# Kernel tuning notes

Hardware: AMD Instinct MI355X
Metric: run time of the kernel (lower is better)

The kernel has to match this reference:

```python
import jax, jax.numpy as jnp
import numpy as np

N_NODES = 50000
N_EDGES = 800000
N_GRAPHS = 512


def gcn_conv(x, W, b, src, dst, n_nodes):
    # Standard PyG GCNConv: linear transform, add self-loops, D^-1/2 (A+I) D^-1/2 aggregation.
    x = x @ W  # [N, out]
    loop = jnp.arange(n_nodes, dtype=src.dtype)
    s = jnp.concatenate([src, loop])  # [E+N]
    d = jnp.concatenate([dst, loop])
    deg = jax.ops.segment_sum(jnp.ones_like(d, dtype=x.dtype), d, num_segments=n_nodes)
    dinv = jnp.where(deg > 0, jax.lax.rsqrt(jnp.maximum(deg, 1e-12)), 0.0)
    norm = dinv[s] * dinv[d]  # [E+N]
    msg = x[s] * norm[:, None]  # gather + scale
    out = jax.ops.segment_sum(msg, d, num_segments=n_nodes)  # scatter-add
    return out + b


def setup_inputs() -> dict:
    key = jax.random.key(0)
    ks = jax.random.split(key, 10)
    x = jax.random.normal(ks[0], (N_NODES, 128), dtype=jnp.float32)
    edge_index = jax.random.randint(ks[1], (2, N_EDGES), 0, N_NODES, dtype=jnp.int64)
    batch = jnp.sort(jax.random.randint(ks[2], (N_NODES,), 0, N_GRAPHS, dtype=jnp.int64))
    y = jax.random.randint(ks[3], (N_GRAPHS,), 0, 4, dtype=jnp.int64)
    W1 = jax.random.normal(ks[4], (128, 64), dtype=jnp.float32) * (1.0 / np.sqrt(128))
    b1 = jnp.zeros((64,), dtype=jnp.float32)
    W2 = jax.random.normal(ks[5], (64, 64), dtype=jnp.float32) * (1.0 / np.sqrt(64))
    b2 = jnp.zeros((64,), dtype=jnp.float32)
    Wfc = jax.random.normal(ks[6], (64, 4), dtype=jnp.float32) * (1.0 / np.sqrt(64))
    bfc = jnp.zeros((4,), dtype=jnp.float32)
    return {"x": x, "edge_index": edge_index, "batch": batch, "y": y,
            "W1": W1, "b1": b1, "W2": W2, "b2": b2, "Wfc": Wfc, "bfc": bfc}


def reference(x, edge_index, batch, y, W1, b1, W2, b2, Wfc, bfc):
    src, dst = edge_index[0], edge_index[1]
    h = jax.nn.relu(gcn_conv(x, W1, b1, src, dst, N_NODES))
    h = jax.nn.relu(gcn_conv(h, W2, b2, src, dst, N_NODES))
    # global mean pool over graph ids
    sums = jax.ops.segment_sum(h, batch, num_segments=N_GRAPHS)  # [G, out]
    cnts = jax.ops.segment_sum(jnp.ones((h.shape[0],), h.dtype), batch, num_segments=N_GRAPHS)
    pooled = sums / jnp.maximum(cnts, 1.0)[:, None]
    logits = pooled @ Wfc + bfc
    logp = jax.nn.log_softmax(logits, axis=1)
    return (logp, y)
```

## Files before the change

### kernel.cpp

```cpp
#include <hip/hip_runtime.h>
#include <hip/hip_fp16.h>
#include <math.h>

#define N_NODES 50000
#define N_EDGES 800000
#define N_GRAPHS 512
#define NBKT 196
#define SENT N_NODES
#define CAP_T 6144
#define CAP_S 8192

typedef float v2f __attribute__((ext_vector_type(2)));

#define OFF_BCNT    0u
#define OFF_DINV    1024u
#define OFF_OFFS2   201216u
#define OFF_TMP     601344u
#define OFF_SORTED  5418240u
#define OFF_XS8_1   11840768u
#define OFF_XS8_2   15041024u
#define OFF_HBUF    18241280u

__global__ __launch_bounds__(256) void binA(const int* __restrict__ src, const int* __restrict__ dst,
                                            int* __restrict__ bcnt, unsigned int* __restrict__ tmp,
                                            unsigned int* __restrict__ x1, unsigned int* __restrict__ x2) {
    __shared__ int cnt[256];
    __shared__ int lo[256];
    __shared__ int cnt2[256];
    __shared__ int baseg[256];
    __shared__ unsigned int ldsPK[4096];
    __shared__ int ldsDST[4096];
    int t = threadIdx.x;
    cnt[t] = 0; cnt2[t] = 0;
    if (blockIdx.x == 0) {
        if (t < 16) x1[N_NODES * 16 + t] = 0;
        else if (t < 32) x2[N_NODES * 16 + (t - 16)] = 0;
    }
    __syncthreads();
    int e0 = blockIdx.x * 4096;
    int nE = N_EDGES - e0; if (nE > 4096) nE = 4096;
    int sA[16], dA[16];
#pragma unroll
    for (int i = 0; i < 16; ++i) {
        int e = e0 + i * 256 + t;
        if (e < N_EDGES) {
            sA[i] = src[e];
            dA[i] = dst[e];
            atomicAdd(&cnt[dA[i] >> 8], 1);
        } else dA[i] = -1;
    }
    __syncthreads();
    {
        int v = cnt[t];
        lo[t] = v;
        __syncthreads();
        for (int d = 1; d < 256; d <<= 1) {
            int a = (t >= d) ? lo[t - d] : 0;
            __syncthreads();
            lo[t] += a;
            __syncthreads();
        }
        int ex = lo[t] - v;
        __syncthreads();
        lo[t] = ex;
        baseg[t] = (t < NBKT && v) ? atomicAdd(&bcnt[t], v) : 0;
    }
    __syncthreads();
#pragma unroll
    for (int i = 0; i < 16; ++i) {
        if (dA[i] >= 0) {
            int b = dA[i] >> 8;
            int pl = lo[b] + atomicAdd(&cnt2[b], 1);
            ldsPK[pl] = (unsigned int)sA[i] | ((unsigned int)(dA[i] & 255) << 17);
            ldsDST[pl] = b * CAP_T + baseg[b] + (pl - lo[b]);
        }
    }
    __syncthreads();
    for (int p = t; p < nE; p += 256)
        tmp[ldsDST[p]] = ldsPK[p];
}

__global__ __launch_bounds__(256) void binB2(const unsigned int* __restrict__ tmp,
                                             const int* __restrict__ bcnt,
                                             int* __restrict__ sorted, int2* __restrict__ offs2,
                                             float* __restrict__ dinv) {
    __shared__ int cnt[256];
    __shared__ int scn[256];
    __shared__ int cur[256];
    __shared__ int ldsS[CAP_S];
    int b = blockIdx.x, t = threadIdx.x;
    cnt[t] = 0;
    __syncthreads();
    int m = bcnt[b];
    const unsigned int* tp = tmp + b * CAP_T;
    for (int e = t; e < m; e += 256) atomicAdd(&cnt[tp[e] >> 17], 1);
    __syncthreads();
    int deg = cnt[t];
    int pdeg = (deg + 7) & ~7;
    scn[t] = pdeg;
    __syncthreads();
    for (int d = 1; d < 256; d <<= 1) {
        int a = (t >= d) ? scn[t - d] : 0;
        __syncthreads();
        scn[t] += a;
        __syncthreads();
    }
    int begl = scn[t] - pdeg;
    int ptot = scn[255];
    int node = b * 256 + t;
    if (node < N_NODES) {
        offs2[node] = make_int2(b * CAP_S + begl, b * CAP_S + begl + pdeg);
        dinv[node] = rsqrtf(1.0f + (float)deg);
    }
    cur[t] = begl;
    __syncthreads();
    for (int e = t; e < m; e += 256) {
        unsigned int pk = tp[e];
        int p = atomicAdd(&cur[pk >> 17], 1);
        ldsS[p] = (int)(pk & 0x1FFFFu);
    }
    __syncthreads();
    for (int p = cur[t]; p < begl + pdeg; ++p) ldsS[p] = SENT;
    __syncthreads();
    int4* dst4 = (int4*)(sorted + b * CAP_S);
    const int4* src4 = (const int4*)ldsS;
    for (int p = t; p < (ptot >> 2); p += 256) dst4[p] = src4[p];
}

__global__ __launch_bounds__(256) void gemm1(const float* __restrict__ X, const float* __restrict__ W,
                                             const float* __restrict__ dinv, unsigned int* __restrict__ xs8) {
    __shared__ float sW[128 * 64];
    __shared__ float sX[16 * 132];
    int tid = threadIdx.x;
    {
        const float4* ws = (const float4*)W;
        float4* wd = (float4*)sW;
        for (int i = tid; i < 2048; i += 256) wd[i] = ws[i];
    }
    int row0 = blockIdx.x * 16;
    {
        const float4* xs = (const float4*)(X + row0 * 128);
        for (int i = tid; i < 512; i += 256) {
            int r = i >> 5, q = i & 31;
            *(float4*)&sX[r * 132 + 4 * q] = xs[r * 32 + q];
        }
    }
    __syncthreads();
    int r = tid >> 4;
    int cg = (tid & 15) * 4;
    int row = row0 + r;
    float a0 = 0, a1 = 0, a2 = 0, a3 = 0;
#pragma unroll 8
    for (int k = 0; k < 128; ++k) {
        float xv = sX[r * 132 + k];
        float4 w = *(const float4*)&sW[k * 64 + cg];
        a0 += xv * w.x; a1 += xv * w.y; a2 += xv * w.z; a3 += xv * w.w;
    }
    float s = dinv[row];
    unsigned int pk = 0;
    pk = __builtin_amdgcn_cvt_pk_fp8_f32(a0 * s, a1 * s, pk, false);
    pk = __builtin_amdgcn_cvt_pk_fp8_f32(a2 * s, a3 * s, pk, true);
    xs8[row * 16 + (cg >> 2)] = pk;
}

__global__ __launch_bounds__(256) void gemm2(const float* __restrict__ X, const float* __restrict__ W,
                                             const float* __restrict__ dinv, unsigned int* __restrict__ xs8) {
    __shared__ float sW[64 * 64];
    __shared__ float sX[16][65];
    int tid = threadIdx.x;
    for (int i = tid; i < 64 * 64; i += 256) sW[i] = W[i];
    int row0 = blockIdx.x * 16;
    for (int i = tid; i < 16 * 64; i += 256) {
        int r = i >> 6, k = i & 63;
        sX[r][k] = X[(row0 + r) * 64 + k];
    }
    __syncthreads();
    int r = tid >> 4;
    int cg = (tid & 15) * 4;
    int row = row0 + r;
    float a0 = 0, a1 = 0, a2 = 0, a3 = 0;
#pragma unroll 8
    for (int k = 0; k < 64; ++k) {
        float xv = sX[r][k];
        float4 w = *(const float4*)&sW[k * 64 + cg];
        a0 += xv * w.x; a1 += xv * w.y; a2 += xv * w.z; a3 += xv * w.w;
    }
    float s = dinv[row];
    unsigned int pk = 0;
    pk = __builtin_amdgcn_cvt_pk_fp8_f32(a0 * s, a1 * s, pk, false);
    pk = __builtin_amdgcn_cvt_pk_fp8_f32(a2 * s, a3 * s, pk, true);
    xs8[row * 16 + (cg >> 2)] = pk;
}

#define ADD_ROW(rv) { \
    v2f f0 = __builtin_amdgcn_cvt_pk_f32_fp8((rv).x, false); \
    v2f f1 = __builtin_amdgcn_cvt_pk_f32_fp8((rv).x, true); \
    v2f f2 = __builtin_amdgcn_cvt_pk_f32_fp8((rv).y, false); \
    v2f f3 = __builtin_amdgcn_cvt_pk_f32_fp8((rv).y, true); \
    a0 += f0.x; a1 += f0.y; a2 += f1.x; a3 += f1.y; \
    a4 += f2.x; a5 += f2.y; a6 += f3.x; a7 += f3.y; }

__global__ __launch_bounds__(256) void gather_m(const unsigned char* __restrict__ xs8,
                                                const int2* __restrict__ offs2,
                                                const int* __restrict__ sorted,
                                                const float* __restrict__ dinv,
                                                const float* __restrict__ bias,
                                                float* __restrict__ fout) {
    int wv = blockIdx.x * 4 + (threadIdx.x >> 6);
    int lane = threadIdx.x & 63;
    int sub = lane >> 3, frag = lane & 7;
    int n0 = wv * 4;
    int2 oe = offs2[n0 + (lane < 4 ? lane : 3)];
    int e0 = __shfl(oe.x, 0), e1 = __shfl(oe.x, 1), e2 = __shfl(oe.x, 2);
    int e3 = __shfl(oe.x, 3), e4 = __shfl(oe.y, 3);
    int G   = (e4 - e0) >> 3;
    int nb1 = (e1 - e0) >> 3, nb2 = (e2 - e0) >> 3, nb3 = (e3 - e0) >> 3;
    const int* sb = sorted + e0 + sub;
    int i0 = (0 < G) ? sb[0]  : SENT;
    int i1 = (1 < G) ? sb[8]  : SENT;
    int i2 = (2 < G) ? sb[16] : SENT;
    int i3 = (3 < G) ? sb[24] : SENT;
    float4 bA = *(const float4*)(bias + frag * 8);
    float4 bB = *(const float4*)(bias + frag * 8 + 4);
    int cur = 0;
    uint2 sv = *(const uint2*)(xs8 + n0 * 64 + frag * 8);
    float dv = dinv[n0];
    float a0 = 0, a1 = 0, a2 = 0, a3 = 0, a4 = 0, a5 = 0, a6 = 0, a7 = 0;

#define FLUSH_ADV() { \
    if (sub == 0) ADD_ROW(sv); \
    a0 += __shfl_xor(a0, 8);  a1 += __shfl_xor(a1, 8);  a2 += __shfl_xor(a2, 8);  a3 += __shfl_xor(a3, 8); \
    a4 += __shfl_xor(a4, 8);  a5 += __shfl_xor(a5, 8);  a6 += __shfl_xor(a6, 8);  a7 += __shfl_xor(a7, 8); \
    a0 += __shfl_xor(a0, 16); a1 += __shfl_xor(a1, 16); a2 += __shfl_xor(a2, 16); a3 += __shfl_xor(a3, 16); \
    a4 += __shfl_xor(a4, 16); a5 += __shfl_xor(a5, 16); a6 += __shfl_xor(a6, 16); a7 += __shfl_xor(a7, 16); \
    a0 += __shfl_xor(a0, 32); a1 += __shfl_xor(a1, 32); a2 += __shfl_xor(a2, 32); a3 += __shfl_xor(a3, 32); \
    a4 += __shfl_xor(a4, 32); a5 += __shfl_xor(a5, 32); a6 += __shfl_xor(a6, 32); a7 += __shfl_xor(a7, 32); \
    if (sub == 0) { \
        float4 w0, w1; \
        w0.x = fmaxf(a0 * dv + bA.x, 0.0f); w0.y = fmaxf(a1 * dv + bA.y, 0.0f); \
        w0.z = fmaxf(a2 * dv + bA.z, 0.0f); w0.w = fmaxf(a3 * dv + bA.w, 0.0f); \
        w1.x = fmaxf(a4 * dv + bB.x, 0.0f); w1.y = fmaxf(a5 * dv + bB.y, 0.0f); \
        w1.z = fmaxf(a6 * dv + bB.z, 0.0f); w1.w = fmaxf(a7 * dv + bB.w, 0.0f); \
        float* o = fout + (n0 + cur) * 64 + frag * 8; \
        *(float4*)(o) = w0; *(float4*)(o + 4) = w1; \
    } \
    a0 = a1 = a2 = a3 = a4 = a5 = a6 = a7 = 0.0f; \
    cur++; \
    if (cur < 4) { \
        sv = *(const uint2*)(xs8 + (n0 + cur) * 64 + frag * 8); \
        dv = dinv[n0 + cur]; \
    } }

#define BND_NXT() (cur == 0 ? nb1 : cur == 1 ? nb2 : cur == 2 ? nb3 : G)

    for (int g = 0; g < G; g += 4) {
        uint2 r0 = *(const uint2*)(xs8 + i0 * 64 + frag * 8);
        uint2 r1 = *(const uint2*)(xs8 + i1 * 64 + frag * 8);
        uint2 r2 = *(const uint2*)(xs8 + i2 * 64 + frag * 8);
        uint2 r3 = *(const uint2*)(xs8 + i3 * 64 + frag * 8);
        const int* np = sb + (g + 4) * 8;
        i0 = (g + 4 < G) ? np[0]  : SENT;
        i1 = (g + 5 < G) ? np[8]  : SENT;
        i2 = (g + 6 < G) ? np[16] : SENT;
        i3 = (g + 7 < G) ? np[24] : SENT;
        {   int gg = g;
            int nxt = BND_NXT();
            while (cur < 4 && gg >= nxt) { FLUSH_ADV(); nxt = BND_NXT(); }
            ADD_ROW(r0); }
        if (g + 1 < G) {
            int gg = g + 1;
            int nxt = BND_NXT();
            while (cur < 4 && gg >= nxt) { FLUSH_ADV(); nxt = BND_NXT(); }
            ADD_ROW(r1);
        }
        if (g + 2 < G) {
            int gg = g + 2;
            int nxt = BND_NXT();
            while (cur < 4 && gg >= nxt) { FLUSH_ADV(); nxt = BND_NXT(); }
            ADD_ROW(r2);
        }
        if (g + 3 < G) {
            int gg = g + 3;
            int nxt = BND_NXT();
            while (cur < 4 && gg >= nxt) { FLUSH_ADV(); nxt = BND_NXT(); }
            ADD_ROW(r3);
        }
    }
    while (cur < 4) { FLUSH_ADV(); }
#undef FLUSH_ADV
#undef BND_NXT
}

__device__ __forceinline__ int lower_bound(const int* __restrict__ a, int n, int v) {
    int lo = 0, hi = n;
    while (lo < hi) { int m = (lo + hi) >> 1; if (a[m] < v) lo = m + 1; else hi = m; }
    return lo;
}

__global__ __launch_bounds__(256) void pool_head(const float* __restrict__ h2,
                                                 const int* __restrict__ batch,
                                                 const float* __restrict__ Wfc, const float* __restrict__ bfc,
                                                 const int* __restrict__ y, float* __restrict__ out) {
    __shared__ int s_beg, s_end;
    __shared__ float sh[4][64];
    __shared__ float pl[64];
    __shared__ float lg[4];
    int g = blockIdx.x;
    int t = threadIdx.x;
    if (t == 0) s_beg = lower_bound(batch, N_NODES, g);
    if (t == 1) s_end = lower_bound(batch, N_NODES, g + 1);
    __syncthreads();
    int beg = s_beg, end = s_end;
    int f = t & 63, seg = t >> 6;
    float s = 0.0f;
    for (int r = beg + seg; r < end; r += 4) s += h2[r * 64 + f];
    sh[seg][f] = s;
    __syncthreads();
    if (t < 64) {
        float p = sh[0][t] + sh[1][t] + sh[2][t] + sh[3][t];
        pl[t] = p / fmaxf((float)(end - beg), 1.0f);
    }
    __syncthreads();
    if (t < 4) {
        float l = bfc[t];
#pragma unroll
        for (int k = 0; k < 64; ++k) l += pl[k] * Wfc[k * 4 + t];
        lg[t] = l;
    }
    __syncthreads();
    if (t == 0) {
        float l0 = lg[0], l1 = lg[1], l2 = lg[2], l3 = lg[3];
        float m = fmaxf(fmaxf(l0, l1), fmaxf(l2, l3));
        float ss = expf(l0 - m) + expf(l1 - m) + expf(l2 - m) + expf(l3 - m);
        float lse = m + logf(ss);
        out[g * 4 + 0] = l0 - lse;
        out[g * 4 + 1] = l1 - lse;
        out[g * 4 + 2] = l2 - lse;
        out[g * 4 + 3] = l3 - lse;
        out[N_GRAPHS * 4 + g] = (float)y[g];
    }
}

extern "C" void kernel_launch(void* const* d_in, const int* in_sizes, int n_in,
                              void* d_out, int out_size, void* d_ws, size_t ws_size,
                              hipStream_t stream) {
    const float* x     = (const float*)d_in[0];
    const int*   ei    = (const int*)d_in[1];
    const int*   batch = (const int*)d_in[2];
    const int*   y     = (const int*)d_in[3];
    const float* W1    = (const float*)d_in[4];
    const float* b1    = (const float*)d_in[5];
    const float* W2    = (const float*)d_in[6];
    const float* b2    = (const float*)d_in[7];
    const float* Wfc   = (const float*)d_in[8];
    const float* bfc   = (const float*)d_in[9];
    float* out = (float*)d_out;

    const int* src = ei;
    const int* dst = ei + N_EDGES;

    char* wsb = (char*)d_ws;
    int*          bcnt   = (int*)(wsb + OFF_BCNT);
    float*        dinv   = (float*)(wsb + OFF_DINV);
    int2*         offs2  = (int2*)(wsb + OFF_OFFS2);
    unsigned int* tmp    = (unsigned int*)(wsb + OFF_TMP);
    int*          sorted = (int*)(wsb + OFF_SORTED);
    unsigned int* xs8_1  = (unsigned int*)(wsb + OFF_XS8_1);
    unsigned int* xs8_2  = (unsigned int*)(wsb + OFF_XS8_2);
    float*        hbuf   = (float*)(wsb + OFF_HBUF);

    hipMemsetAsync(bcnt, 0, 1024u, stream);

    binA<<<NBKT, 256, 0, stream>>>(src, dst, bcnt, tmp, xs8_1, xs8_2);
    binB2<<<NBKT, 256, 0, stream>>>(tmp, bcnt, sorted, offs2, dinv);

    gemm1<<<N_NODES / 16, 256, 0, stream>>>(x, W1, dinv, xs8_1);
    gather_m<<<N_NODES / 16, 256, 0, stream>>>((const unsigned char*)xs8_1, offs2, sorted, dinv, b1, hbuf);
    gemm2<<<N_NODES / 16, 256, 0, stream>>>(hbuf, W2, dinv, xs8_2);
    gather_m<<<N_NODES / 16, 256, 0, stream>>>((const unsigned char*)xs8_2, offs2, sorted, dinv, b2, hbuf);

    pool_head<<<N_GRAPHS, 256, 0, stream>>>(hbuf, batch, Wfc, bfc, y, out);
}
```

Baseline: 204.9 us.

## Fuse layer-1 aggregation with layer-2 GEMM and store final activations as fp16

```diff
diff --git a/kernel.cpp b/kernel.cpp
--- a/kernel.cpp
+++ b/kernel.cpp
@@ -19,7 +19,7 @@
 #define OFF_SORTED  5418240u
 #define OFF_XS8_1   11840768u
 #define OFF_XS8_2   15041024u
-#define OFF_HBUF    18241280u
+#define OFF_H2      18241280u
 
 __global__ __launch_bounds__(256) void binA(const int* __restrict__ src, const int* __restrict__ dst,
                                             int* __restrict__ bcnt, unsigned int* __restrict__ tmp,
@@ -163,35 +163,6 @@
     xs8[row * 16 + (cg >> 2)] = pk;
 }
 
-__global__ __launch_bounds__(256) void gemm2(const float* __restrict__ X, const float* __restrict__ W,
-                                             const float* __restrict__ dinv, unsigned int* __restrict__ xs8) {
-    __shared__ float sW[64 * 64];
-    __shared__ float sX[16][65];
-    int tid = threadIdx.x;
-    for (int i = tid; i < 64 * 64; i += 256) sW[i] = W[i];
-    int row0 = blockIdx.x * 16;
-    for (int i = tid; i < 16 * 64; i += 256) {
-        int r = i >> 6, k = i & 63;
-        sX[r][k] = X[(row0 + r) * 64 + k];
-    }
-    __syncthreads();
-    int r = tid >> 4;
-    int cg = (tid & 15) * 4;
-    int row = row0 + r;
-    float a0 = 0, a1 = 0, a2 = 0, a3 = 0;
-#pragma unroll 8
-    for (int k = 0; k < 64; ++k) {
-        float xv = sX[r][k];
-        float4 w = *(const float4*)&sW[k * 64 + cg];
-        a0 += xv * w.x; a1 += xv * w.y; a2 += xv * w.z; a3 += xv * w.w;
-    }
-    float s = dinv[row];
-    unsigned int pk = 0;
-    pk = __builtin_amdgcn_cvt_pk_fp8_f32(a0 * s, a1 * s, pk, false);
-    pk = __builtin_amdgcn_cvt_pk_fp8_f32(a2 * s, a3 * s, pk, true);
-    xs8[row * 16 + (cg >> 2)] = pk;
-}
-
 #define ADD_ROW(rv) { \
     v2f f0 = __builtin_amdgcn_cvt_pk_f32_fp8((rv).x, false); \
     v2f f1 = __builtin_amdgcn_cvt_pk_f32_fp8((rv).x, true); \
@@ -200,49 +171,99 @@
     a0 += f0.x; a1 += f0.y; a2 += f1.x; a3 += f1.y; \
     a4 += f2.x; a5 += f2.y; a6 += f3.x; a7 += f3.y; }
 
-__global__ __launch_bounds__(256) void gather_m(const unsigned char* __restrict__ xs8,
-                                                const int2* __restrict__ offs2,
-                                                const int* __restrict__ sorted,
-                                                const float* __restrict__ dinv,
-                                                const float* __restrict__ bias,
-                                                float* __restrict__ fout) {
-    int wv = blockIdx.x * 4 + (threadIdx.x >> 6);
-    int lane = threadIdx.x & 63;
-    int sub = lane >> 3, frag = lane & 7;
-    int n0 = wv * 4;
-    int2 oe = offs2[n0 + (lane < 4 ? lane : 3)];
-    int e0 = __shfl(oe.x, 0), e1 = __shfl(oe.x, 1), e2 = __shfl(oe.x, 2);
-    int e3 = __shfl(oe.x, 3), e4 = __shfl(oe.y, 3);
-    int G   = (e4 - e0) >> 3;
-    int nb1 = (e1 - e0) >> 3, nb2 = (e2 - e0) >> 3, nb3 = (e3 - e0) >> 3;
-    const int* sb = sorted + e0 + sub;
-    int i0 = (0 < G) ? sb[0]  : SENT;
-    int i1 = (1 < G) ? sb[8]  : SENT;
-    int i2 = (2 < G) ? sb[16] : SENT;
-    int i3 = (3 < G) ? sb[24] : SENT;
-    float4 bA = *(const float4*)(bias + frag * 8);
-    float4 bB = *(const float4*)(bias + frag * 8 + 4);
-    int cur = 0;
-    uint2 sv = *(const uint2*)(xs8 + n0 * 64 + frag * 8);
-    float dv = dinv[n0];
-    float a0 = 0, a1 = 0, a2 = 0, a3 = 0, a4 = 0, a5 = 0, a6 = 0, a7 = 0;
-
-#define FLUSH_ADV() { \
-    if (sub == 0) ADD_ROW(sv); \
+#define RED_SUB() { \
     a0 += __shfl_xor(a0, 8);  a1 += __shfl_xor(a1, 8);  a2 += __shfl_xor(a2, 8);  a3 += __shfl_xor(a3, 8); \
     a4 += __shfl_xor(a4, 8);  a5 += __shfl_xor(a5, 8);  a6 += __shfl_xor(a6, 8);  a7 += __shfl_xor(a7, 8); \
     a0 += __shfl_xor(a0, 16); a1 += __shfl_xor(a1, 16); a2 += __shfl_xor(a2, 16); a3 += __shfl_xor(a3, 16); \
     a4 += __shfl_xor(a4, 16); a5 += __shfl_xor(a5, 16); a6 += __shfl_xor(a6, 16); a7 += __shfl_xor(a7, 16); \
     a0 += __shfl_xor(a0, 32); a1 += __shfl_xor(a1, 32); a2 += __shfl_xor(a2, 32); a3 += __shfl_xor(a3, 32); \
-    a4 += __shfl_xor(a4, 32); a5 += __shfl_xor(a5, 32); a6 += __shfl_xor(a6, 32); a7 += __shfl_xor(a7, 32); \
+    a4 += __shfl_xor(a4, 32); a5 += __shfl_xor(a5, 32); a6 += __shfl_xor(a6, 32); a7 += __shfl_xor(a7, 32); }
+
+#define GATHER_BODY(FLUSH_ADV) \
+    int lane = threadIdx.x & 63; \
+    int sub = lane >> 3, frag = lane & 7; \
+    int n0 = wv * 4; \
+    int2 oe = offs2[n0 + (lane < 4 ? lane : 3)]; \
+    int e0 = __shfl(oe.x, 0), e1 = __shfl(oe.x, 1), e2 = __shfl(oe.x, 2); \
+    int e3 = __shfl(oe.x, 3), e4 = __shfl(oe.y, 3); \
+    int G   = (e4 - e0) >> 3; \
+    int nb1 = (e1 - e0) >> 3, nb2 = (e2 - e0) >> 3, nb3 = (e3 - e0) >> 3; \
+    const int* sb = sorted + e0 + sub; \
+    int i0 = (0 < G) ? sb[0]  : SENT; \
+    int i1 = (1 < G) ? sb[8]  : SENT; \
+    int i2 = (2 < G) ? sb[16] : SENT; \
+    int i3 = (3 < G) ? sb[24] : SENT; \
+    float4 bA = *(const float4*)(bias + frag * 8); \
+    float4 bB = *(const float4*)(bias + frag * 8 + 4); \
+    int cur = 0; \
+    uint2 sv = *(const uint2*)(xs8 + n0 * 64 + frag * 8); \
+    float dv = dinv[n0]; \
+    float a0 = 0, a1 = 0, a2 = 0, a3 = 0, a4 = 0, a5 = 0, a6 = 0, a7 = 0; \
+    for (int g = 0; g < G; g += 4) { \
+        uint2 r0 = *(const uint2*)(xs8 + i0 * 64 + frag * 8); \
+        uint2 r1 = *(const uint2*)(xs8 + i1 * 64 + frag * 8); \
+        uint2 r2 = *(const uint2*)(xs8 + i2 * 64 + frag * 8); \
+        uint2 r3 = *(const uint2*)(xs8 + i3 * 64 + frag * 8); \
+        const int* np = sb + (g + 4) * 8; \
+        i0 = (g + 4 < G) ? np[0]  : SENT; \
+        i1 = (g + 5 < G) ? np[8]  : SENT; \
+        i2 = (g + 6 < G) ? np[16] : SENT; \
+        i3 = (g + 7 < G) ? np[24] : SENT; \
+        {   int gg = g; \
+            int nxt = BND_NXT(); \
+            while (cur < 4 && gg >= nxt) { FLUSH_ADV(); nxt = BND_NXT(); } \
+            ADD_ROW(r0); } \
+        if (g + 1 < G) { \
+            int gg = g + 1; \
+            int nxt = BND_NXT(); \
+            while (cur < 4 && gg >= nxt) { FLUSH_ADV(); nxt = BND_NXT(); } \
+            ADD_ROW(r1); \
+        } \
+        if (g + 2 < G) { \
+            int gg = g + 2; \
+            int nxt = BND_NXT(); \
+            while (cur < 4 && gg >= nxt) { FLUSH_ADV(); nxt = BND_NXT(); } \
+            ADD_ROW(r2); \
+        } \
+        if (g + 3 < G) { \
+            int gg = g + 3; \
+            int nxt = BND_NXT(); \
+            while (cur < 4 && gg >= nxt) { FLUSH_ADV(); nxt = BND_NXT(); } \
+            ADD_ROW(r3); \
+        } \
+    } \
+    while (cur < 4) { FLUSH_ADV(); }
+
+#define BND_NXT() (cur == 0 ? nb1 : cur == 1 ? nb2 : cur == 2 ? nb3 : G)
+
+__global__ __launch_bounds__(256) void gather_fuse(const unsigned char* __restrict__ xs8,
+                                                   const int2* __restrict__ offs2,
+                                                   const int* __restrict__ sorted,
+                                                   const float* __restrict__ dinv,
+                                                   const float* __restrict__ bias,
+                                                   const float* __restrict__ W2,
+                                                   unsigned int* __restrict__ xs8o) {
+    __shared__ float sW2[64 * 64];
+    __shared__ float sH[16][64];
+    {
+        const float4* ws = (const float4*)W2;
+        float4* wd = (float4*)sW2;
+        for (int i = threadIdx.x; i < 1024; i += 256) wd[i] = ws[i];
+    }
+    int wvl = threadIdx.x >> 6;
+    int wv = blockIdx.x * 4 + wvl;
+
+#define FLUSH_LDS() { \
+    if (sub == 0) ADD_ROW(sv); \
+    RED_SUB(); \
     if (sub == 0) { \
         float4 w0, w1; \
         w0.x = fmaxf(a0 * dv + bA.x, 0.0f); w0.y = fmaxf(a1 * dv + bA.y, 0.0f); \
         w0.z = fmaxf(a2 * dv + bA.z, 0.0f); w0.w = fmaxf(a3 * dv + bA.w, 0.0f); \
         w1.x = fmaxf(a4 * dv + bB.x, 0.0f); w1.y = fmaxf(a5 * dv + bB.y, 0.0f); \
         w1.z = fmaxf(a6 * dv + bB.z, 0.0f); w1.w = fmaxf(a7 * dv + bB.w, 0.0f); \
-        float* o = fout + (n0 + cur) * 64 + frag * 8; \
-        *(float4*)(o) = w0; *(float4*)(o + 4) = w1; \
+        *(float4*)&sH[wvl * 4 + cur][frag * 8]     = w0; \
+        *(float4*)&sH[wvl * 4 + cur][frag * 8 + 4] = w1; \
     } \
     a0 = a1 = a2 = a3 = a4 = a5 = a6 = a7 = 0.0f; \
     cur++; \
@@ -251,44 +272,58 @@
         dv = dinv[n0 + cur]; \
     } }
 
-#define BND_NXT() (cur == 0 ? nb1 : cur == 1 ? nb2 : cur == 2 ? nb3 : G)
-
-    for (int g = 0; g < G; g += 4) {
-        uint2 r0 = *(const uint2*)(xs8 + i0 * 64 + frag * 8);
-        uint2 r1 = *(const uint2*)(xs8 + i1 * 64 + frag * 8);
-        uint2 r2 = *(const uint2*)(xs8 + i2 * 64 + frag * 8);
-        uint2 r3 = *(const uint2*)(xs8 + i3 * 64 + frag * 8);
-        const int* np = sb + (g + 4) * 8;
-        i0 = (g + 4 < G) ? np[0]  : SENT;
-        i1 = (g + 5 < G) ? np[8]  : SENT;
-        i2 = (g + 6 < G) ? np[16] : SENT;
-        i3 = (g + 7 < G) ? np[24] : SENT;
-        {   int gg = g;
-            int nxt = BND_NXT();
-            while (cur < 4 && gg >= nxt) { FLUSH_ADV(); nxt = BND_NXT(); }
-            ADD_ROW(r0); }
-        if (g + 1 < G) {
-            int gg = g + 1;
-            int nxt = BND_NXT();
-            while (cur < 4 && gg >= nxt) { FLUSH_ADV(); nxt = BND_NXT(); }
-            ADD_ROW(r1);
-        }
-        if (g + 2 < G) {
-            int gg = g + 2;
-            int nxt = BND_NXT();
-            while (cur < 4 && gg >= nxt) { FLUSH_ADV(); nxt = BND_NXT(); }
-            ADD_ROW(r2);
-        }
-        if (g + 3 < G) {
-            int gg = g + 3;
-            int nxt = BND_NXT();
-            while (cur < 4 && gg >= nxt) { FLUSH_ADV(); nxt = BND_NXT(); }
-            ADD_ROW(r3);
-        }
-    }
-    while (cur < 4) { FLUSH_ADV(); }
-#undef FLUSH_ADV
-#undef BND_NXT
+    GATHER_BODY(FLUSH_LDS)
+#undef FLUSH_LDS
+    __syncthreads();
+    int r = threadIdx.x >> 4;
+    int cg = (threadIdx.x & 15) * 4;
+    int node = blockIdx.x * 16 + r;
+    float b0 = 0, b1 = 0, b2 = 0, b3 = 0;
+#pragma unroll 8
+    for (int k = 0; k < 64; ++k) {
+        float hv = sH[r][k];
+        float4 w = *(const float4*)&sW2[k * 64 + cg];
+        b0 += hv * w.x; b1 += hv * w.y; b2 += hv * w.z; b3 += hv * w.w;
+    }
+    float s = dinv[node];
+    unsigned int pk = 0;
+    pk = __builtin_amdgcn_cvt_pk_fp8_f32(b0 * s, b1 * s, pk, false);
+    pk = __builtin_amdgcn_cvt_pk_fp8_f32(b2 * s, b3 * s, pk, true);
+    xs8o[node * 16 + (cg >> 2)] = pk;
+}
+
+__global__ __launch_bounds__(256) void gather_h2(const unsigned char* __restrict__ xs8,
+                                                 const int2* __restrict__ offs2,
+                                                 const int* __restrict__ sorted,
+                                                 const float* __restrict__ dinv,
+                                                 const float* __restrict__ bias,
+                                                 __half* __restrict__ h2) {
+    int wv = blockIdx.x * 4 + (threadIdx.x >> 6);
+
+#define FLUSH_H2() { \
+    if (sub == 0) ADD_ROW(sv); \
+    RED_SUB(); \
+    if (sub == 0) { \
+        float v0 = fmaxf(a0 * dv + bA.x, 0.0f), v1 = fmaxf(a1 * dv + bA.y, 0.0f); \
+        float v2 = fmaxf(a2 * dv + bA.z, 0.0f), v3 = fmaxf(a3 * dv + bA.w, 0.0f); \
+        float v4 = fmaxf(a4 * dv + bB.x, 0.0f), v5 = fmaxf(a5 * dv + bB.y, 0.0f); \
+        float v6 = fmaxf(a6 * dv + bB.z, 0.0f), v7 = fmaxf(a7 * dv + bB.w, 0.0f); \
+        __half2 p0 = __floats2half2_rn(v0, v1), p1 = __floats2half2_rn(v2, v3); \
+        __half2 p2 = __floats2half2_rn(v4, v5), p3 = __floats2half2_rn(v6, v7); \
+        uint4 pk; \
+        pk.x = *(unsigned int*)&p0; pk.y = *(unsigned int*)&p1; \
+        pk.z = *(unsigned int*)&p2; pk.w = *(unsigned int*)&p3; \
+        *(uint4*)(h2 + (n0 + cur) * 64 + frag * 8) = pk; \
+    } \
+    a0 = a1 = a2 = a3 = a4 = a5 = a6 = a7 = 0.0f; \
+    cur++; \
+    if (cur < 4) { \
+        sv = *(const uint2*)(xs8 + (n0 + cur) * 64 + frag * 8); \
+        dv = dinv[n0 + cur]; \
+    } }
+
+    GATHER_BODY(FLUSH_H2)
+#undef FLUSH_H2
 }
 
 __device__ __forceinline__ int lower_bound(const int* __restrict__ a, int n, int v) {
@@ -297,7 +332,7 @@
     return lo;
 }
 
-__global__ __launch_bounds__(256) void pool_head(const float* __restrict__ h2,
+__global__ __launch_bounds__(256) void pool_head(const __half* __restrict__ h2,
                                                  const int* __restrict__ batch,
                                                  const float* __restrict__ Wfc, const float* __restrict__ bfc,
                                                  const int* __restrict__ y, float* __restrict__ out) {
@@ -313,7 +348,7 @@
     int beg = s_beg, end = s_end;
     int f = t & 63, seg = t >> 6;
     float s = 0.0f;
-    for (int r = beg + seg; r < end; r += 4) s += h2[r * 64 + f];
+    for (int r = beg + seg; r < end; r += 4) s += __half2float(h2[r * 64 + f]);
     sh[seg][f] = s;
     __syncthreads();
     if (t < 64) {
@@ -367,7 +402,7 @@
     int*          sorted = (int*)(wsb + OFF_SORTED);
     unsigned int* xs8_1  = (unsigned int*)(wsb + OFF_XS8_1);
     unsigned int* xs8_2  = (unsigned int*)(wsb + OFF_XS8_2);
-    float*        hbuf   = (float*)(wsb + OFF_HBUF);
+    __half*       h2     = (__half*)(wsb + OFF_H2);
 
     hipMemsetAsync(bcnt, 0, 1024u, stream);
 
@@ -375,9 +410,10 @@
     binB2<<<NBKT, 256, 0, stream>>>(tmp, bcnt, sorted, offs2, dinv);
 
     gemm1<<<N_NODES / 16, 256, 0, stream>>>(x, W1, dinv, xs8_1);
-    gather_m<<<N_NODES / 16, 256, 0, stream>>>((const unsigned char*)xs8_1, offs2, sorted, dinv, b1, hbuf);
-    gemm2<<<N_NODES / 16, 256, 0, stream>>>(hbuf, W2, dinv, xs8_2);
-    gather_m<<<N_NODES / 16, 256, 0, stream>>>((const unsigned char*)xs8_2, offs2, sorted, dinv, b2, hbuf);
-
-    pool_head<<<N_GRAPHS, 256, 0, stream>>>(hbuf, batch, Wfc, bfc, y, out);
-}
+    gather_fuse<<<N_NODES / 16, 256, 0, stream>>>((const unsigned char*)xs8_1, offs2, sorted,
+                                                  dinv, b1, W2, xs8_2);
+    gather_h2<<<N_NODES / 16, 256, 0, stream>>>((const unsigned char*)xs8_2, offs2, sorted,
+                                                dinv, b2, h2);
+
+    pool_head<<<N_GRAPHS, 256, 0, stream>>>(h2, batch, Wfc, bfc, y, out);
+}
```

After: 196.7 us, median of 2. 1.04x faster.
